# Performance work log

Measured on AMD Instinct MI355X. Metric: run time of the kernel, lower is better.

## Reference

```python
import jax, jax.numpy as jnp
import numpy as np
import math

HEADS = 16
HIDDEN = 2048
D_K = HIDDEN // HEADS
BATCH = 2
SEQ = 2048
ROPE_THETA = 10000.0


def make_freqs_cis(seq_len, d_k, theta=ROPE_THETA):
    # Llama rotary frequencies; returned as (seq, d_k//2, 2) = (cos, sin)
    inv_freq = 1.0 / (theta ** (np.arange(0, d_k, 2, dtype=np.float32) / d_k))
    t = np.arange(seq_len, dtype=np.float32)
    ang = np.outer(t, inv_freq)  # (seq, d_k//2)
    return jnp.asarray(np.stack([np.cos(ang), np.sin(ang)], axis=-1))


def setup_inputs() -> dict:
    key = jax.random.key(0)
    ks = jax.random.split(key, 5)
    scale = 1.0 / math.sqrt(HIDDEN)
    return {
        "x": jax.random.normal(ks[0], (BATCH, SEQ, HIDDEN), dtype=jnp.float32),
        "freqs_cis": make_freqs_cis(SEQ, D_K),
        "wq": jax.random.normal(ks[1], (HIDDEN, HIDDEN), dtype=jnp.float32) * scale,
        "wk": jax.random.normal(ks[2], (HIDDEN, HIDDEN), dtype=jnp.float32) * scale,
        "wv": jax.random.normal(ks[3], (HIDDEN, HIDDEN), dtype=jnp.float32) * scale,
        "wo": jax.random.normal(ks[4], (HIDDEN, HIDDEN), dtype=jnp.float32) * scale,
    }


def _apply_rope(t, cos, sin):
    # t: (B, S, h, d_k); cos/sin: (1, S, 1, d_k//2)
    B, S, h, dk = t.shape
    tp = t.reshape(B, S, h, dk // 2, 2)
    t0, t1 = tp[..., 0], tp[..., 1]
    r0 = t0 * cos - t1 * sin
    r1 = t0 * sin + t1 * cos
    return jnp.stack([r0, r1], axis=-1).reshape(B, S, h, dk)


def reference(x, freqs_cis, wq, wk, wv, wo):
    B, S, H = x.shape
    h, dk = HEADS, H // HEADS
    # nn.Linear(bias=False): y = x @ W.T
    q = (x @ wq.T).reshape(B, S, h, dk)
    k = (x @ wk.T).reshape(B, S, h, dk)
    v = (x @ wv.T).reshape(B, S, h, dk)
    cos = freqs_cis[None, :, None, :, 0]
    sin = freqs_cis[None, :, None, :, 1]
    q = _apply_rope(q, cos, sin)
    k = _apply_rope(k, cos, sin)
    # (B, h, S, dk)
    q = q.transpose(0, 2, 1, 3)
    k = k.transpose(0, 2, 1, 3)
    v = v.transpose(0, 2, 1, 3)
    scores = jnp.einsum("bhqd,bhkd->bhqk", q, k) / math.sqrt(dk)
    causal = jnp.tril(jnp.ones((S, S), dtype=bool))
    scores = jnp.where(causal[None, None], scores, -jnp.inf)
    attn = jax.nn.softmax(scores, axis=-1)
    out = jnp.einsum("bhqk,bhkd->bhqd", attn, v)
    out = out.transpose(0, 2, 1, 3).reshape(B, S, H)
    return out @ wo.T
```

## Files before the change

### kernel.cpp

```cpp
#include <hip/hip_runtime.h>

#define SEQ 2048
#define HID 2048
#define NH 16
#define DK 128
#define NTOK 4096

typedef __bf16 bf16x8 __attribute__((ext_vector_type(8)));
typedef float f32x4 __attribute__((ext_vector_type(4)));
typedef float f32x16 __attribute__((ext_vector_type(16)));
typedef unsigned int u32x4 __attribute__((ext_vector_type(4)));

__device__ __forceinline__ unsigned short f2bf(float f) {
  unsigned int u = __builtin_bit_cast(unsigned int, f);
  u += 0x7fffu + ((u >> 16) & 1u);
  return (unsigned short)(u >> 16);
}
__device__ __forceinline__ float bf2f(unsigned int lo16) {
  return __builtin_bit_cast(float, lo16 << 16);
}

__device__ __forceinline__ void async_cp16(const void* g, void* l) {
  __builtin_amdgcn_global_load_lds(
      (__attribute__((address_space(1))) void*)const_cast<void*>(g),
      (__attribute__((address_space(3))) void*)l, 16, 0, 0);
}

__global__ void convert_all_kernel(const float* __restrict__ x,
                                   const float* __restrict__ wq,
                                   const float* __restrict__ wk,
                                   const float* __restrict__ wv,
                                   const float* __restrict__ wo,
                                   const float* __restrict__ fc,
                                   unsigned short* __restrict__ xb,
                                   unsigned short* __restrict__ wqb,
                                   unsigned short* __restrict__ wkb,
                                   unsigned short* __restrict__ wvb,
                                   unsigned short* __restrict__ wob,
                                   unsigned int* __restrict__ fcb) {
  const int bid = blockIdx.x;
  if (bid >= 24576) {
    const int idx = (bid - 24576) * 256 + threadIdx.x;
    const int s = idx >> 6, d = idx & 63;
    const float2 cs = *(const float2*)(fc + s * 128 + 2 * d);
    fcb[idx] = (unsigned int)f2bf(cs.x) | ((unsigned int)f2bf(cs.y) << 16);
    return;
  }
  const float* src;
  unsigned short* dst;
  int base;
  if (bid < 8192) {
    src = x; dst = xb; base = bid;
  } else {
    const int t = (bid - 8192) >> 12;
    base = (bid - 8192) & 4095;
    src = (t == 0) ? wq : (t == 1) ? wk : (t == 2) ? wv : wo;
    dst = (t == 0) ? wqb : (t == 1) ? wkb : (t == 2) ? wvb : wob;
  }
  const int i = base * 256 + threadIdx.x;
  float4 v = ((const float4*)src)[i];
  ushort4 o;
  o.x = f2bf(v.x); o.y = f2bf(v.y); o.z = f2bf(v.z); o.w = f2bf(v.w);
  ((ushort4*)dst)[i] = o;
}

template<bool F32OUT>
__global__ __launch_bounds__(256, 2)
void gemm_bt_kernel(const unsigned short* __restrict__ A,
                    const unsigned short* __restrict__ B0,
                    const unsigned short* __restrict__ B1,
                    const unsigned short* __restrict__ B2,
                    unsigned short* __restrict__ O0,
                    unsigned short* __restrict__ O1,
                    unsigned short* __restrict__ O2,
                    float* __restrict__ Of,
                    const unsigned int* __restrict__ fcb) {
  __shared__ alignas(16) unsigned short As[128 * 64];
  __shared__ alignas(16) unsigned short Bs[128 * 64];

  const int bx = blockIdx.x, by = blockIdx.y;
  const unsigned short* B;
  unsigned short* Ob = nullptr;
  int sel = 0, col0;
  if (F32OUT) {
    B = B0;
    col0 = bx * 128;
  } else {
    sel = bx >> 4;
    B = (sel == 0) ? B0 : (sel == 1) ? B1 : B2;
    Ob = (sel == 0) ? O0 : (sel == 1) ? O1 : O2;
    col0 = (bx & 15) * 128;
  }
  const int row0 = by * 128;

  const int tid = threadIdx.x;
  const int wave = tid >> 6, lane = tid & 63;
  const int quad = lane >> 4, r = lane & 15;
  const int wm = wave >> 1, wn = wave & 1;
  const int jbase = wave * 256 + lane;

  f32x4 acc[4][4] = {};

  for (int k0 = 0; k0 < HID; k0 += 64) {
    for (int t = 0; t < 4; ++t) {
      const int j = jbase + t * 64;
      const int m = j >> 3;
      const int gc = (j & 7) ^ (m & 7);
      async_cp16(A + (size_t)(row0 + m) * HID + k0 + gc * 8, As + j * 8);
      async_cp16(B + (size_t)(col0 + m) * HID + k0 + gc * 8, Bs + j * 8);
    }
    __syncthreads();
    for (int kk = 0; kk < 2; ++kk) {
      bf16x8 af[4], bfr[4];
      for (int mt = 0; mt < 4; ++mt) {
        const int m = wm * 64 + mt * 16 + r;
        const int slot = (kk * 4 + quad) ^ (m & 7);
        af[mt] = __builtin_bit_cast(bf16x8, *(const u32x4*)(As + m * 64 + slot * 8));
      }
      for (int nt = 0; nt < 4; ++nt) {
        const int n = wn * 64 + nt * 16 + r;
        const int slot = (kk * 4 + quad) ^ (n & 7);
        bfr[nt] = __builtin_bit_cast(bf16x8, *(const u32x4*)(Bs + n * 64 + slot * 8));
      }
      for (int mt = 0; mt < 4; ++mt)
        for (int nt = 0; nt < 4; ++nt)
          acc[mt][nt] = __builtin_amdgcn_mfma_f32_16x16x32_bf16(
              af[mt], bfr[nt], acc[mt][nt], 0, 0, 0);
    }
    __syncthreads();
  }

  if (!F32OUT && sel == 2) {
    for (int mt = 0; mt < 4; ++mt) {
      const int row = row0 + wm * 64 + mt * 16 + quad * 4;
      const int b = row >> 11, s = row & (SEQ - 1);
      for (int nt = 0; nt < 4; ++nt) {
        const int col = col0 + wn * 64 + nt * 16 + r;
        ushort4 pk;
        pk.x = f2bf(acc[mt][nt][0]);
        pk.y = f2bf(acc[mt][nt][1]);
        pk.z = f2bf(acc[mt][nt][2]);
        pk.w = f2bf(acc[mt][nt][3]);
        *(ushort4*)(Ob + ((size_t)(b * HID + col)) * SEQ + s) = pk;
      }
    }
    return;
  }

  if (!F32OUT) {
    const float qs = (sel == 0) ? 0.12751743f : 1.0f;
    for (int mt = 0; mt < 4; ++mt) {
      const int row = row0 + wm * 64 + mt * 16 + quad * 4;
      for (int nt = 0; nt < 4; ++nt) {
        const int col = col0 + wn * 64 + nt * 16 + r;
        const int d = (wn * 64 + nt * 16 + r) >> 1;
        for (int v = 0; v < 4; ++v) {
          const int s = (row + v) & (SEQ - 1);
          const unsigned int u = fcb[s * 64 + d];
          const float c = bf2f(u & 0xffffu), sn = bf2f(u >> 16);
          const float val = acc[mt][nt][v];
          const float par = __shfl_xor(val, 1, 64);
          const float res = (r & 1) ? (par * sn + val * c)
                                    : (val * c - par * sn);
          Ob[(size_t)(row + v) * HID + col] = f2bf(res * qs);
        }
      }
    }
    return;
  }

  for (int mt = 0; mt < 4; ++mt) {
    const int row = row0 + wm * 64 + mt * 16 + quad * 4;
    for (int nt = 0; nt < 4; ++nt) {
      const int col = col0 + wn * 64 + nt * 16 + r;
      for (int v = 0; v < 4; ++v)
        Of[(size_t)(row + v) * HID + col] = acc[mt][nt][v];
    }
  }
}

__global__ __launch_bounds__(256, 2)
void flash_attn_kernel(const unsigned short* __restrict__ Qb,
                       const unsigned short* __restrict__ Kb,
                       const unsigned short* __restrict__ VtG,
                       unsigned short* __restrict__ Ob) {
  __shared__ alignas(16) unsigned short KsA[64 * 128];
  __shared__ alignas(16) unsigned short KsB[64 * 128];
  __shared__ alignas(16) unsigned short VsA[128 * 64];
  __shared__ alignas(16) unsigned short VsB[128 * 64];

  const int bx = blockIdx.x, bh = blockIdx.y;
  const int tid = threadIdx.x, wave = tid >> 6, lane = tid & 63;
  const int l31 = lane & 31, hl = lane >> 5;
  const int qgrp = wave >> 1, ksub = wave & 1;
  const int tokbase = (bh >> 4) * SEQ;
  const int hh = bh & 15;

  auto stage = [&](int kt, unsigned short* Ks, unsigned short* Vs) {
    for (int t = 0; t < 4; ++t) {
      const int j = t * 256 + tid;
      const int n = j >> 4, slot = j & 15;
      const int gc = slot ^ (n & 15);
      async_cp16(Kb + (size_t)(tokbase + kt * 64 + n) * HID + hh * DK + gc * 8,
                 Ks + j * 8);
    }
    for (int t = 0; t < 4; ++t) {
      const int j = t * 256 + tid;
      const int d = j >> 3, slot = j & 7;
      const int gc = slot ^ (d & 7);
      async_cp16(VtG + ((size_t)(bh * DK + d)) * SEQ + kt * 64 + gc * 8,
                 Vs + j * 8);
    }
  };

  for (int phase = 0; phase < 2; ++phase) {
    const int qt = phase ? (31 - bx) : bx;
    const int q0 = qt * 64;
    const int qloc = qgrp * 32 + l31;

    u32x4 qf[8];
    {
      const unsigned short* qrow =
          Qb + (size_t)(tokbase + q0 + qloc) * HID + hh * DK;
#pragma unroll
      for (int ks = 0; ks < 8; ++ks)
        qf[ks] = *(const u32x4*)(qrow + ks * 16 + hl * 8);
    }

    f32x16 o[4] = {};
    float m_i = -__builtin_inff(), l_i = 0.f;

    auto body = [&](const unsigned short* Ks, const unsigned short* Vs,
                    int kt) {
      f32x16 s = {};
      const unsigned short* krow = Ks + (size_t)(ksub * 32 + l31) * 128;
      __builtin_amdgcn_s_setprio(1);
#pragma unroll
      for (int ks = 0; ks < 8; ++ks) {
        const int slot = (ks * 2 + hl) ^ (lane & 15);
        const u32x4 kf = *(const u32x4*)(krow + slot * 8);
        s = __builtin_amdgcn_mfma_f32_32x32x16_bf16(
            __builtin_bit_cast(bf16x8, kf),
            __builtin_bit_cast(bf16x8, qf[ks]), s, 0, 0, 0);
      }
      __builtin_amdgcn_s_setprio(0);

      float sv[16];
#pragma unroll
      for (int r = 0; r < 16; ++r) sv[r] = s[r];
      if (kt == qt) {
#pragma unroll
        for (int r = 0; r < 16; ++r) {
          const int kloc = ksub * 32 + (r & 3) + 8 * (r >> 2) + 4 * hl;
          if (kloc > qloc) sv[r] = -__builtin_inff();
        }
      }

      float mx = fmaxf(fmaxf(fmaxf(sv[0], sv[1]), fmaxf(sv[2], sv[3])),
                       fmaxf(fmaxf(sv[4], sv[5]), fmaxf(sv[6], sv[7])));
      mx = fmaxf(mx,
                 fmaxf(fmaxf(fmaxf(sv[8], sv[9]), fmaxf(sv[10], sv[11])),
                       fmaxf(fmaxf(sv[12], sv[13]), fmaxf(sv[14], sv[15]))));
      mx = fmaxf(mx, __shfl_xor(mx, 32, 64));

      if (!__all(mx <= m_i + 8.f)) {
        const float mnew = fmaxf(m_i, mx);
        const float al = exp2f(m_i - mnew);
        m_i = mnew;
        l_i *= al;
#pragma unroll
        for (int dt = 0; dt < 4; ++dt)
#pragma unroll
          for (int r = 0; r < 16; ++r) o[dt][r] *= al;
      }

      float p[16];
      float rs = 0.f;
#pragma unroll
      for (int r = 0; r < 16; ++r) {
        p[r] = exp2f(fmaxf(sv[r] - m_i, -128.f));
        rs += p[r];
      }
      l_i += rs + __shfl_xor(rs, 32, 64);

      u32x4 af[2];
#pragma unroll
      for (int kk = 0; kk < 2; ++kk) {
        unsigned int a, b2, c2, d2;
        asm("v_cvt_pk_bf16_f32 %0, %1, %2"
            : "=v"(a) : "v"(p[8 * kk + 0]), "v"(p[8 * kk + 1]));
        asm("v_cvt_pk_bf16_f32 %0, %1, %2"
            : "=v"(b2) : "v"(p[8 * kk + 2]), "v"(p[8 * kk + 3]));
        asm("v_cvt_pk_bf16_f32 %0, %1, %2"
            : "=v"(c2) : "v"(p[8 * kk + 4]), "v"(p[8 * kk + 5]));
        asm("v_cvt_pk_bf16_f32 %0, %1, %2"
            : "=v"(d2) : "v"(p[8 * kk + 6]), "v"(p[8 * kk + 7]));
        asm("v_permlane32_swap_b32 %0, %1" : "+v"(a), "+v"(c2));
        asm("v_permlane32_swap_b32 %0, %1" : "+v"(b2), "+v"(d2));
        u32x4 t = {a, b2, c2, d2};
        af[kk] = t;
      }

      __builtin_amdgcn_s_setprio(1);
#pragma unroll
      for (int kk = 0; kk < 2; ++kk)
#pragma unroll
        for (int dt = 0; dt < 4; ++dt) {
          const int d = dt * 32 + l31;
          const int slot = (ksub * 4 + kk * 2 + hl) ^ (d & 7);
          const u32x4 vv = *(const u32x4*)(Vs + (size_t)d * 64 + slot * 8);
          o[dt] = __builtin_amdgcn_mfma_f32_32x32x16_bf16(
              __builtin_bit_cast(bf16x8, af[kk]),
              __builtin_bit_cast(bf16x8, vv), o[dt], 0, 0, 0);
        }
      __builtin_amdgcn_s_setprio(0);
    };

    stage(0, KsA, VsA);
    int kt = 0;
    while (true) {
      __syncthreads();
      if (kt + 1 <= qt) stage(kt + 1, KsB, VsB);
      body(KsA, VsA, kt);
      if (++kt > qt) break;
      __syncthreads();
      if (kt + 1 <= qt) stage(kt + 1, KsA, VsA);
      body(KsB, VsB, kt);
      if (++kt > qt) break;
    }

    __syncthreads();
    float* obuf = (float*)(qgrp == 0 ? (void*)KsA : (void*)VsA);
    float* mlbuf = (float*)KsB;
    if (ksub == 1) {
#pragma unroll
      for (int dt = 0; dt < 4; ++dt)
#pragma unroll
        for (int r = 0; r < 16; ++r) {
          const int qr = (r & 3) + 8 * (r >> 2) + 4 * hl;
          obuf[qr * 128 + dt * 32 + l31] = o[dt][r];
        }
    }
    if (lane < 32) {
      mlbuf[wave * 64 + lane] = m_i;
      mlbuf[wave * 64 + 32 + lane] = l_i;
    }
    __syncthreads();
    if (ksub == 0) {
      float f0[16], f1[16];
#pragma unroll
      for (int r = 0; r < 16; ++r) {
        const int qr = (r & 3) + 8 * (r >> 2) + 4 * hl;
        const float m0 = mlbuf[wave * 64 + qr];
        const float l0 = mlbuf[wave * 64 + 32 + qr];
        const float m1 = mlbuf[(wave + 1) * 64 + qr];
        const float l1 = mlbuf[(wave + 1) * 64 + 32 + qr];
        const float mm = fmaxf(m0, m1);
        const float a0 = exp2f(fmaxf(m0 - mm, -128.f));
        const float a1 = exp2f(fmaxf(m1 - mm, -128.f));
        const float li = 1.f / (l0 * a0 + l1 * a1);
        f0[r] = a0 * li;
        f1[r] = a1 * li;
      }
#pragma unroll
      for (int dt = 0; dt < 4; ++dt)
#pragma unroll
        for (int r = 0; r < 16; ++r) {
          const int qr = (r & 3) + 8 * (r >> 2) + 4 * hl;
          const float om =
              o[dt][r] * f0[r] + obuf[qr * 128 + dt * 32 + l31] * f1[r];
          Ob[(size_t)(tokbase + q0 + qgrp * 32 + qr) * HID + hh * DK +
             dt * 32 + l31] = f2bf(om);
        }
    }
    __syncthreads();
  }
}

extern "C" void kernel_launch(void* const* d_in, const int* in_sizes, int n_in,
                              void* d_out, int out_size, void* d_ws, size_t ws_size,
                              hipStream_t stream) {
  const float* x  = (const float*)d_in[0];
  const float* fc = (const float*)d_in[1];
  const float* wq = (const float*)d_in[2];
  const float* wk = (const float*)d_in[3];
  const float* wv = (const float*)d_in[4];
  const float* wo = (const float*)d_in[5];
  float* out = (float*)d_out;

  unsigned short* xb  = (unsigned short*)d_ws;
  unsigned short* wqb = xb  + (size_t)NTOK * HID;
  unsigned short* wkb = wqb + (size_t)HID * HID;
  unsigned short* wvb = wkb + (size_t)HID * HID;
  unsigned short* wob = wvb + (size_t)HID * HID;
  unsigned short* qb  = wob + (size_t)HID * HID;
  unsigned short* kb  = qb  + (size_t)NTOK * HID;
  unsigned short* vtb = kb  + (size_t)NTOK * HID;
  unsigned short* ab  = vtb + (size_t)NTOK * HID;
  unsigned int*   fcb = (unsigned int*)(ab + (size_t)NTOK * HID);

  convert_all_kernel<<<24576 + 512, 256, 0, stream>>>(
      x, wq, wk, wv, wo, fc, xb, wqb, wkb, wvb, wob, fcb);

  gemm_bt_kernel<false><<<dim3(48, 32), 256, 0, stream>>>(
      xb, wqb, wkb, wvb, qb, kb, vtb, nullptr, fcb);

  flash_attn_kernel<<<dim3(16, 32), 256, 0, stream>>>(qb, kb, vtb, ab);

  gemm_bt_kernel<true><<<dim3(16, 32), 256, 0, stream>>>(
      ab, wob, nullptr, nullptr, nullptr, nullptr, nullptr, out, fcb);
}
```

Before: 372.0 us.

## Split fused QKV GEMM into three launches and remap attention block order

Replaces the single 48x32-block QKV projection launch with three separate 16x32 launches, one per weight, passing the output mode as a runtime argument. The flash attention kernel now remaps linear block IDs so consecutive blocks are spread across the 8 groups, which interleaves heavy and light causal tiles and may change how work lands on XCDs and caches. Separate launches simplify per-block pointer selection but add launch overhead and drop any overlap between the three projections inside one grid.

New measurement: 376.9 us. No clear change (+1.3%).

```diff
diff --git a/kernel.cpp b/kernel.cpp
--- a/kernel.cpp
+++ b/kernel.cpp
@@ -67,30 +67,16 @@
 template<bool F32OUT>
 __global__ __launch_bounds__(256, 2)
 void gemm_bt_kernel(const unsigned short* __restrict__ A,
-                    const unsigned short* __restrict__ B0,
-                    const unsigned short* __restrict__ B1,
-                    const unsigned short* __restrict__ B2,
-                    unsigned short* __restrict__ O0,
-                    unsigned short* __restrict__ O1,
-                    unsigned short* __restrict__ O2,
+                    const unsigned short* __restrict__ B,
+                    unsigned short* __restrict__ Ob,
                     float* __restrict__ Of,
-                    const unsigned int* __restrict__ fcb) {
+                    const unsigned int* __restrict__ fcb,
+                    const int mode) {
   __shared__ alignas(16) unsigned short As[128 * 64];
   __shared__ alignas(16) unsigned short Bs[128 * 64];
 
   const int bx = blockIdx.x, by = blockIdx.y;
-  const unsigned short* B;
-  unsigned short* Ob = nullptr;
-  int sel = 0, col0;
-  if (F32OUT) {
-    B = B0;
-    col0 = bx * 128;
-  } else {
-    sel = bx >> 4;
-    B = (sel == 0) ? B0 : (sel == 1) ? B1 : B2;
-    Ob = (sel == 0) ? O0 : (sel == 1) ? O1 : O2;
-    col0 = (bx & 15) * 128;
-  }
+  const int col0 = bx * 128;
   const int row0 = by * 128;
 
   const int tid = threadIdx.x;
@@ -130,7 +116,7 @@
     __syncthreads();
   }
 
-  if (!F32OUT && sel == 2) {
+  if (!F32OUT && mode == 2) {
     for (int mt = 0; mt < 4; ++mt) {
       const int row = row0 + wm * 64 + mt * 16 + quad * 4;
       const int b = row >> 11, s = row & (SEQ - 1);
@@ -148,7 +134,7 @@
   }
 
   if (!F32OUT) {
-    const float qs = (sel == 0) ? 0.12751743f : 1.0f;
+    const float qs = (mode == 0) ? 0.12751743f : 1.0f;
     for (int mt = 0; mt < 4; ++mt) {
       const int row = row0 + wm * 64 + mt * 16 + quad * 4;
       for (int nt = 0; nt < 4; ++nt) {
@@ -189,7 +175,9 @@
   __shared__ alignas(16) unsigned short VsA[128 * 64];
   __shared__ alignas(16) unsigned short VsB[128 * 64];
 
-  const int bx = blockIdx.x, bh = blockIdx.y;
+  const int bid0 = blockIdx.y * 16 + blockIdx.x;
+  const int wid = (bid0 & 7) * 64 + (bid0 >> 3);
+  const int bx = wid & 15, bh = wid >> 4;
   const int tid = threadIdx.x, wave = tid >> 6, lane = tid & 63;
   const int l31 = lane & 31, hl = lane >> 5;
   const int qgrp = wave >> 1, ksub = wave & 1;
@@ -402,11 +390,15 @@
   convert_all_kernel<<<24576 + 512, 256, 0, stream>>>(
       x, wq, wk, wv, wo, fc, xb, wqb, wkb, wvb, wob, fcb);
 
-  gemm_bt_kernel<false><<<dim3(48, 32), 256, 0, stream>>>(
-      xb, wqb, wkb, wvb, qb, kb, vtb, nullptr, fcb);
+  gemm_bt_kernel<false><<<dim3(16, 32), 256, 0, stream>>>(
+      xb, wqb, qb, nullptr, fcb, 0);
+  gemm_bt_kernel<false><<<dim3(16, 32), 256, 0, stream>>>(
+      xb, wkb, kb, nullptr, fcb, 1);
+  gemm_bt_kernel<false><<<dim3(16, 32), 256, 0, stream>>>(
+      xb, wvb, vtb, nullptr, fcb, 2);
 
   flash_attn_kernel<<<dim3(16, 32), 256, 0, stream>>>(qb, kb, vtb, ab);
 
   gemm_bt_kernel<true><<<dim3(16, 32), 256, 0, stream>>>(
-      ab, wob, nullptr, nullptr, nullptr, nullptr, nullptr, out, fcb);
-}
+      ab, wob, nullptr, out, fcb, 0);
+}
```
